# Performance work log

Hardware: AMD Instinct MI355X
Metric: run time of the kernel (lower is better)

## Reference

```python
import jax, jax.numpy as jnp
import numpy as np

B, T, E, H = 4, 2048, 1024, 16
HS = E // H  # 64
EPS = 1e-5


def _layernorm(x, g, b):
    mu = jnp.mean(x, axis=-1, keepdims=True)
    var = jnp.mean(jnp.square(x - mu), axis=-1, keepdims=True)
    return (x - mu) * jax.lax.rsqrt(var + EPS) * g + b


def setup_inputs() -> dict:
    key = jax.random.key(0)
    ks = jax.random.split(key, 12)
    s = 0.02
    return {
        "x": jax.random.normal(ks[0], (B, T, E), dtype=jnp.float32),
        "ln1_g": jnp.ones((E,), jnp.float32),
        "ln1_b": jnp.zeros((E,), jnp.float32),
        "Wq": jax.random.normal(ks[1], (H, E, HS), jnp.float32) * s,
        "Wk": jax.random.normal(ks[2], (H, E, HS), jnp.float32) * s,
        "Wv": jax.random.normal(ks[3], (H, E, HS), jnp.float32) * s,
        "Wo": jax.random.normal(ks[4], (E, E), jnp.float32) * s,
        "bo": jnp.zeros((E,), jnp.float32),
        "ln2_g": jnp.ones((E,), jnp.float32),
        "ln2_b": jnp.zeros((E,), jnp.float32),
        "W1": jax.random.normal(ks[5], (E, 4 * E), jnp.float32) * s,
        "b1": jnp.zeros((4 * E,), jnp.float32),
        "W2": jax.random.normal(ks[6], (4 * E, E), jnp.float32) * s,
        "b2": jnp.zeros((E,), jnp.float32),
    }


def reference(x, ln1_g, ln1_b, Wq, Wk, Wv, Wo, bo, ln2_g, ln2_b, W1, b1, W2, b2):
    # --- self-attention (pre-LN) ---
    h = _layernorm(x, ln1_g, ln1_b)                      # [B,T,E]
    q = jnp.einsum('bte,hed->bhtd', h, Wq)               # [B,H,T,HS]
    k = jnp.einsum('bte,hed->bhtd', h, Wk)
    v = jnp.einsum('bte,hed->bhtd', h, Wv)
    scores = jnp.einsum('bhtd,bhsd->bhts', q, k) * (HS ** -0.5)  # [B,H,T,T]
    att = jax.nn.softmax(scores, axis=-1)
    o = jnp.einsum('bhts,bhsd->bhtd', att, v)            # [B,H,T,HS]
    o = jnp.transpose(o, (0, 2, 1, 3)).reshape(B, T, E)  # concat heads
    x = x + o @ Wo + bo                                  # residual
    # --- feed-forward (pre-LN) ---
    h2 = _layernorm(x, ln2_g, ln2_b)
    x = x + jax.nn.relu(h2 @ W1 + b1) @ W2 + b2
    return x
```

## Files before the change

### kernel.cpp

```cpp
#include <hip/hip_runtime.h>
#include <stdint.h>


typedef __attribute__((ext_vector_type(8))) short s16x8;
typedef __attribute__((ext_vector_type(4))) float f32x4;
typedef unsigned short u16;
typedef __attribute__((ext_vector_type(4))) unsigned short u16x4;

__device__ __forceinline__ u16 f2bf(float f) {
    uint32_t u = __float_as_uint(f);
    u += 0x7fffu + ((u >> 16) & 1u);
    return (u16)(u >> 16);
}

__global__ __launch_bounds__(256)
void ln_bf16(const float* __restrict__ x, const float* __restrict__ g,
             const float* __restrict__ bta, u16* __restrict__ y) {
    __shared__ float red[8];
    const int row = blockIdx.x;
    const int t = threadIdx.x;
    const float4 xv = ((const float4*)(x + (size_t)row * 1024))[t];
    float s = xv.x + xv.y + xv.z + xv.w;
    float q = xv.x*xv.x + xv.y*xv.y + xv.z*xv.z + xv.w*xv.w;
#pragma unroll
    for (int off = 32; off; off >>= 1) {
        s += __shfl_down(s, off, 64);
        q += __shfl_down(q, off, 64);
    }
    if ((t & 63) == 0) { red[(t>>6)*2] = s; red[(t>>6)*2+1] = q; }
    __syncthreads();
    const float st = red[0]+red[2]+red[4]+red[6];
    const float qt = red[1]+red[3]+red[5]+red[7];
    const float mu = st * (1.f/1024.f);
    const float rs = rsqrtf(qt*(1.f/1024.f) - mu*mu + 1e-5f);
    const float4 gv = ((const float4*)g)[t];
    const float4 bv = ((const float4*)bta)[t];
    u16x4 o;
    o.x = f2bf((xv.x-mu)*rs*gv.x + bv.x);
    o.y = f2bf((xv.y-mu)*rs*gv.y + bv.y);
    o.z = f2bf((xv.z-mu)*rs*gv.z + bv.z);
    o.w = f2bf((xv.w-mu)*rs*gv.w + bv.w);
    ((u16x4*)(y + (size_t)row*1024))[t] = o;
}

__global__ __launch_bounds__(256)
void transpose_f32_bf16(const float* __restrict__ in, u16* __restrict__ out,
                        int K, int N) {
    __shared__ float tile[64][65];
    const int k0 = blockIdx.x * 64;
    const int n0 = blockIdx.y * 64;
    const int t = threadIdx.x;
    const int r = t >> 2;
    const int c = (t & 3) * 16;
    const float* ip = in + (size_t)(k0 + r) * N + n0 + c;
#pragma unroll
    for (int i = 0; i < 4; ++i) {
        const float4 v = *(const float4*)(ip + i*4);
        tile[r][c+i*4+0]=v.x; tile[r][c+i*4+1]=v.y;
        tile[r][c+i*4+2]=v.z; tile[r][c+i*4+3]=v.w;
    }
    __syncthreads();
    u16 tmp[16] __attribute__((aligned(16)));
#pragma unroll
    for (int i = 0; i < 16; ++i) tmp[i] = f2bf(tile[c+i][r]);
    u16* op = out + (size_t)(n0 + r) * K + k0 + c;
    *(s16x8*)op       = *(const s16x8*)&tmp[0];
    *(s16x8*)(op + 8) = *(const s16x8*)&tmp[8];
}

__global__ __launch_bounds__(256)
void pack_wcat(const float* __restrict__ Wq, const float* __restrict__ Wk,
               const float* __restrict__ Wv, u16* __restrict__ out) {
    __shared__ float tile[64][65];
    const int ph = blockIdx.y;
    const int p = ph >> 4, h = ph & 15;
    const float* W = (p == 0) ? Wq : (p == 1 ? Wk : Wv);
    const float* in = W + (size_t)h * 64 * 1024;
    const int k0 = blockIdx.x * 64;
    const int t = threadIdx.x;
    const int r = t >> 2;
    const int c = (t & 3) * 16;
    const float* ip = in + (size_t)(k0 + r) * 64 + c;
#pragma unroll
    for (int i = 0; i < 4; ++i) {
        const float4 v = *(const float4*)(ip + i*4);
        tile[r][c+i*4+0]=v.x; tile[r][c+i*4+1]=v.y;
        tile[r][c+i*4+2]=v.z; tile[r][c+i*4+3]=v.w;
    }
    __syncthreads();
    u16 tmp[16] __attribute__((aligned(16)));
#pragma unroll
    for (int i = 0; i < 16; ++i) tmp[i] = f2bf(tile[c+i][r]);
    u16* op = out + (size_t)(p*1024 + h*64 + r) * 1024 + k0 + c;
    *(s16x8*)op       = *(const s16x8*)&tmp[0];
    *(s16x8*)(op + 8) = *(const s16x8*)&tmp[8];
}

template<bool RELU, bool HAS_BIAS, bool HAS_RES, bool OUT_BF16>
__global__ __launch_bounds__(256, 2)
void bgemm(const u16* __restrict__ A, int lda,
           const u16* __restrict__ Bt, int ldb,
           void* __restrict__ Cv, int ldc,
           const float* __restrict__ bias,
           const float* __restrict__ Res, int ldres, int K)
{
    __shared__ u16 Als[128*64];
    __shared__ u16 Bls[128*64];
    const int tid = threadIdx.x;
    const int wid = tid >> 6, lane = tid & 63;
    const int bm = blockIdx.y * 128, bn = blockIdx.x * 128;
    const int wr = (wid >> 1) * 64, wc = (wid & 1) * 64;
    const int srow = tid >> 3;
    const int sce  = (tid & 7) * 8;
    const int fr = lane & 15, fq = lane >> 4;

    const f32x4 zero = {0.f, 0.f, 0.f, 0.f};
    f32x4 acc[4][4];
#pragma unroll
    for (int m = 0; m < 4; ++m)
#pragma unroll
        for (int n = 0; n < 4; ++n) acc[m][n] = zero;

    const u16* Ap = A  + (size_t)(bm + srow) * lda + sce;
    const u16* Bp = Bt + (size_t)(bn + srow) * ldb + sce;
    const size_t a32 = (size_t)32 * lda, b32 = (size_t)32 * ldb;

    int wb[4];
#pragma unroll
    for (int c2 = 0; c2 < 4; ++c2) {
        const int row = c2*32 + srow;
        wb[c2] = row*128 + (((tid & 7) * 16) ^ ((row & 7) << 4));
    }

    s16x8 ar[4], br[4];
#pragma unroll
    for (int c2 = 0; c2 < 4; ++c2) {
        ar[c2] = *(const s16x8*)(Ap + c2*a32);
        br[c2] = *(const s16x8*)(Bp + c2*b32);
    }

    for (int k0 = 0; k0 < K; k0 += 64) {
        __syncthreads();
#pragma unroll
        for (int c2 = 0; c2 < 4; ++c2) {
            *(s16x8*)((char*)Als + wb[c2]) = ar[c2];
            *(s16x8*)((char*)Bls + wb[c2]) = br[c2];
        }
        __syncthreads();
        if (k0 + 64 < K) {
#pragma unroll
            for (int c2 = 0; c2 < 4; ++c2) {
                ar[c2] = *(const s16x8*)(Ap + (k0 + 64) + c2*a32);
                br[c2] = *(const s16x8*)(Bp + (k0 + 64) + c2*b32);
            }
        }
#pragma unroll
        for (int kk = 0; kk < 2; ++kk) {
            s16x8 af[4], bf[4];
#pragma unroll
            for (int m = 0; m < 4; ++m) {
                const int r = wr + m*16 + fr;
                const int cb = (kk*64 + fq*16) ^ ((r & 7) << 4);
                af[m] = *(const s16x8*)((const char*)Als + r*128 + cb);
            }
#pragma unroll
            for (int n = 0; n < 4; ++n) {
                const int r = wc + n*16 + fr;
                const int cb = (kk*64 + fq*16) ^ ((r & 7) << 4);
                bf[n] = *(const s16x8*)((const char*)Bls + r*128 + cb);
            }
#pragma unroll
            for (int m = 0; m < 4; ++m)
#pragma unroll
                for (int n = 0; n < 4; ++n)
                    acc[m][n] = __builtin_amdgcn_mfma_f32_16x16x32_bf16(
                        af[m], bf[n], acc[m][n], 0, 0, 0);
        }
    }

    float* Cf = (float*)Cv;
    u16*  Cb = (u16*)Cv;
#pragma unroll
    for (int n = 0; n < 4; ++n) {
        const int col = bn + wc + n*16 + fr;
        const float bval = HAS_BIAS ? bias[col] : 0.f;
#pragma unroll
        for (int m = 0; m < 4; ++m) {
#pragma unroll
            for (int j = 0; j < 4; ++j) {
                const int row = bm + wr + m*16 + fq*4 + j;
                float v = acc[m][n][j] + bval;
                if (HAS_RES) v += Res[(size_t)row * ldres + col];
                if (RELU)    v = fmaxf(v, 0.f);
                if (OUT_BF16) Cb[(size_t)row * ldc + col] = f2bf(v);
                else          Cf[(size_t)row * ldc + col] = v;
            }
        }
    }
}

__global__ __launch_bounds__(256)
void attn_bf16(const u16* __restrict__ qkv, u16* __restrict__ out) {
    __shared__ u16 Qs[64*72];
    __shared__ u16 Ks[64*72];
    __shared__ u16 Vt[64*72];
    __shared__ u16 Ps[64*72];
    const int b = blockIdx.y >> 4, h = blockIdx.y & 15;
    const int q0 = blockIdx.x << 6;
    const int tid = threadIdx.x;
    const int wid = tid >> 6, lane = tid & 63;
    const int fr = lane & 15, fq = lane >> 4;
    const int srow = tid >> 2;
    const int sce  = (tid & 3) * 16;
    const size_t tokbase = (size_t)b * 2048;

    {
        const u16* qp = qkv + (tokbase + q0 + srow) * 3072 + h*64 + sce;
        *(s16x8*)&Qs[srow*72 + sce]     = *(const s16x8*)qp;
        *(s16x8*)&Qs[srow*72 + sce + 8] = *(const s16x8*)(qp + 8);
    }
    const s16x8 qf0 = *(const s16x8*)&Qs[(wid*16 + fr)*72 + fq*8];
    const s16x8 qf1 = *(const s16x8*)&Qs[(wid*16 + fr)*72 + 32 + fq*8];

    float m_run[4] = {-3e38f, -3e38f, -3e38f, -3e38f};
    float l_run[4] = {0.f, 0.f, 0.f, 0.f};
    const f32x4 zero = {0.f, 0.f, 0.f, 0.f};
    f32x4 oacc[4];
#pragma unroll
    for (int nd = 0; nd < 4; ++nd) oacc[nd] = zero;

    for (int kt = 0; kt < 2048; kt += 64) {
        const u16* kp = qkv + (tokbase + kt + srow)*3072 + 1024 + h*64 + sce;
        const s16x8 kv0 = *(const s16x8*)kp;
        const s16x8 kv1 = *(const s16x8*)(kp + 8);
        const s16x8 vv0 = *(const s16x8*)(kp + 1024);
        const s16x8 vv1 = *(const s16x8*)(kp + 1032);
        __syncthreads();
        *(s16x8*)&Ks[srow*72 + sce]     = kv0;
        *(s16x8*)&Ks[srow*72 + sce + 8] = kv1;
#pragma unroll
        for (int i = 0; i < 8; ++i) {
            Vt[(sce + i)*72 + srow]     = (u16)vv0[i];
            Vt[(sce + i + 8)*72 + srow] = (u16)vv1[i];
        }
        __syncthreads();

        f32x4 sv[4];
#pragma unroll
        for (int n = 0; n < 4; ++n) sv[n] = zero;
#pragma unroll
        for (int n = 0; n < 4; ++n) {
            const s16x8 kf0 = *(const s16x8*)&Ks[(n*16 + fr)*72 + fq*8];
            const s16x8 kf1 = *(const s16x8*)&Ks[(n*16 + fr)*72 + 32 + fq*8];
            sv[n] = __builtin_amdgcn_mfma_f32_16x16x32_bf16(qf0, kf0, sv[n], 0,0,0);
            sv[n] = __builtin_amdgcn_mfma_f32_16x16x32_bf16(qf1, kf1, sv[n], 0,0,0);
        }

#pragma unroll
        for (int j = 0; j < 4; ++j) {
            const float s0 = sv[0][j]*0.125f, s1 = sv[1][j]*0.125f;
            const float s2 = sv[2][j]*0.125f, s3 = sv[3][j]*0.125f;
            float mx = fmaxf(fmaxf(s0, s1), fmaxf(s2, s3));
#pragma unroll
            for (int off = 1; off < 16; off <<= 1)
                mx = fmaxf(mx, __shfl_xor(mx, off, 64));
            const float mn = fmaxf(m_run[j], mx);
            const float al = __expf(m_run[j] - mn);
            m_run[j] = mn;
            const float p0 = __expf(s0 - mn), p1 = __expf(s1 - mn);
            const float p2 = __expf(s2 - mn), p3 = __expf(s3 - mn);
            float rs = p0 + p1 + p2 + p3;
#pragma unroll
            for (int off = 1; off < 16; off <<= 1)
                rs += __shfl_xor(rs, off, 64);
            l_run[j] = l_run[j]*al + rs;
#pragma unroll
            for (int nd = 0; nd < 4; ++nd) oacc[nd][j] *= al;
            const int prow = (wid*16 + fq*4 + j)*72;
            Ps[prow + fr]      = f2bf(p0);
            Ps[prow + 16 + fr] = f2bf(p1);
            Ps[prow + 32 + fr] = f2bf(p2);
            Ps[prow + 48 + fr] = f2bf(p3);
        }

        const s16x8 pf0 = *(const s16x8*)&Ps[(wid*16 + fr)*72 + fq*8];
        const s16x8 pf1 = *(const s16x8*)&Ps[(wid*16 + fr)*72 + 32 + fq*8];
#pragma unroll
        for (int nd = 0; nd < 4; ++nd) {
            const s16x8 vf0 = *(const s16x8*)&Vt[(nd*16 + fr)*72 + fq*8];
            const s16x8 vf1 = *(const s16x8*)&Vt[(nd*16 + fr)*72 + 32 + fq*8];
            oacc[nd] = __builtin_amdgcn_mfma_f32_16x16x32_bf16(pf0, vf0, oacc[nd], 0,0,0);
            oacc[nd] = __builtin_amdgcn_mfma_f32_16x16x32_bf16(pf1, vf1, oacc[nd], 0,0,0);
        }
    }

#pragma unroll
    for (int j = 0; j < 4; ++j) {
        const float inv = 1.0f / l_run[j];
        const size_t row = tokbase + q0 + wid*16 + fq*4 + j;
#pragma unroll
        for (int nd = 0; nd < 4; ++nd)
            out[row*1024 + h*64 + nd*16 + fr] = f2bf(oacc[nd][j] * inv);
    }
}

extern "C" void kernel_launch(void* const* d_in, const int* in_sizes, int n_in,
                              void* d_out, int out_size, void* d_ws, size_t ws_size,
                              hipStream_t stream) {
    (void)in_sizes; (void)n_in; (void)out_size; (void)ws_size;
    const float* x     = (const float*)d_in[0];
    const float* ln1_g = (const float*)d_in[1];
    const float* ln1_b = (const float*)d_in[2];
    const float* Wq    = (const float*)d_in[3];
    const float* Wk    = (const float*)d_in[4];
    const float* Wv    = (const float*)d_in[5];
    const float* Wo    = (const float*)d_in[6];
    const float* bo    = (const float*)d_in[7];
    const float* ln2_g = (const float*)d_in[8];
    const float* ln2_b = (const float*)d_in[9];
    const float* W1    = (const float*)d_in[10];
    const float* b1    = (const float*)d_in[11];
    const float* W2    = (const float*)d_in[12];
    const float* b2    = (const float*)d_in[13];
    float* out = (float*)d_out;

    char* w = (char*)d_ws;
    u16* WcatT = (u16*)w;  w += (size_t)3072*1024*2;
    u16* WoT   = (u16*)w;  w += (size_t)1024*1024*2;
    u16* W1T   = (u16*)w;  w += (size_t)4096*1024*2;
    u16* W2T   = (u16*)w;  w += (size_t)1024*4096*2;
    u16* hb    = (u16*)w;  w += (size_t)8192*1024*2;
    u16* qkvb  = (u16*)w;  w += (size_t)8192*3072*2;
    u16* attno = (u16*)w;  w += (size_t)8192*1024*2;
    u16* a1    = (u16*)w;  w += (size_t)8192*4096*2;

    pack_wcat<<<dim3(16, 48), 256, 0, stream>>>(Wq, Wk, Wv, WcatT);
    transpose_f32_bf16<<<dim3(16, 16), 256, 0, stream>>>(Wo, WoT, 1024, 1024);
    transpose_f32_bf16<<<dim3(16, 64), 256, 0, stream>>>(W1, W1T, 1024, 4096);
    transpose_f32_bf16<<<dim3(64, 16), 256, 0, stream>>>(W2, W2T, 4096, 1024);

    ln_bf16<<<dim3(8192), 256, 0, stream>>>(x, ln1_g, ln1_b, hb);
    bgemm<false,false,false,true><<<dim3(24, 64), 256, 0, stream>>>(
        hb, 1024, WcatT, 1024, qkvb, 3072, nullptr, nullptr, 0, 1024);
    attn_bf16<<<dim3(32, 64), 256, 0, stream>>>(qkvb, attno);
    bgemm<false,true,true,false><<<dim3(8, 64), 256, 0, stream>>>(
        attno, 1024, WoT, 1024, out, 1024, bo, x, 1024, 1024);
    ln_bf16<<<dim3(8192), 256, 0, stream>>>(out, ln2_g, ln2_b, hb);
    bgemm<true,true,false,true><<<dim3(32, 64), 256, 0, stream>>>(
        hb, 1024, W1T, 1024, a1, 4096, b1, nullptr, 0, 1024);
    bgemm<false,true,true,false><<<dim3(8, 64), 256, 0, stream>>>(
        a1, 4096, W2T, 4096, out, 1024, b2, out, 1024, 4096);
}
```

Baseline: 718.0 us.

## Use direct global-to-LDS loads in GEMM and restructure attention with transposed scores

The GEMM now loads A/B tiles straight into LDS with global_load_lds, dropping the register staging, the XOR swizzle and the register prefetch, and relaxes launch bounds. Attention moves to 128-key tiles with swizzled LDS layouts and computes S^T (K times Q), so each lane owns a single query row. This removes most of the cross-lane shuffles in the softmax, and the 1/8 scale is folded into Q once. The aim is less LDS bank conflict and reduction overhead in attention and less staging cost in the GEMM, but the GEMM loses its load/compute overlap and may now see unswizzled LDS read conflicts.

New measurement: 634.6 us. 1.13x faster.

```diff
diff --git a/kernel.cpp b/kernel.cpp
--- a/kernel.cpp
+++ b/kernel.cpp
@@ -7,10 +7,24 @@
 typedef unsigned short u16;
 typedef __attribute__((ext_vector_type(4))) unsigned short u16x4;
 
+#define XSW(r) ((((r) & 7) ^ (((r) >> 3) & 7)) << 4)
+
 __device__ __forceinline__ u16 f2bf(float f) {
     uint32_t u = __float_as_uint(f);
     u += 0x7fffu + ((u >> 16) & 1u);
     return (u16)(u >> 16);
+}
+__device__ __forceinline__ float bf2f(u16 u) {
+    return __uint_as_float(((uint32_t)u) << 16);
+}
+__device__ __forceinline__ uint32_t pk2(float a, float b) {
+    return (uint32_t)f2bf(a) | ((uint32_t)f2bf(b) << 16);
+}
+
+__device__ __forceinline__ void gld16(const void* g, void* l) {
+    __builtin_amdgcn_global_load_lds(
+        (const __attribute__((address_space(1))) unsigned int*)g,
+        (__attribute__((address_space(3))) unsigned int*)l, 16, 0, 0);
 }
 
 __global__ __launch_bounds__(256)
@@ -97,12 +111,12 @@
 }
 
 template<bool RELU, bool HAS_BIAS, bool HAS_RES, bool OUT_BF16>
-__global__ __launch_bounds__(256, 2)
+__global__ __launch_bounds__(256)
 void bgemm(const u16* __restrict__ A, int lda,
            const u16* __restrict__ Bt, int ldb,
-           void* __restrict__ Cv, int ldc,
+           void* Cv, int ldc,
            const float* __restrict__ bias,
-           const float* __restrict__ Res, int ldres, int K)
+           const float* Res, int ldres, int K)
 {
     __shared__ u16 Als[128*64];
     __shared__ u16 Bls[128*64];
@@ -110,9 +124,8 @@
     const int wid = tid >> 6, lane = tid & 63;
     const int bm = blockIdx.y * 128, bn = blockIdx.x * 128;
     const int wr = (wid >> 1) * 64, wc = (wid & 1) * 64;
-    const int srow = tid >> 3;
-    const int sce  = (tid & 7) * 8;
     const int fr = lane & 15, fq = lane >> 4;
+    const int sr8 = lane >> 3, sc8 = (lane & 7) * 8;
 
     const f32x4 zero = {0.f, 0.f, 0.f, 0.f};
     f32x4 acc[4][4];
@@ -121,54 +134,27 @@
 #pragma unroll
         for (int n = 0; n < 4; ++n) acc[m][n] = zero;
 
-    const u16* Ap = A  + (size_t)(bm + srow) * lda + sce;
-    const u16* Bp = Bt + (size_t)(bn + srow) * ldb + sce;
-    const size_t a32 = (size_t)32 * lda, b32 = (size_t)32 * ldb;
-
-    int wb[4];
-#pragma unroll
-    for (int c2 = 0; c2 < 4; ++c2) {
-        const int row = c2*32 + srow;
-        wb[c2] = row*128 + (((tid & 7) * 16) ^ ((row & 7) << 4));
-    }
-
-    s16x8 ar[4], br[4];
-#pragma unroll
-    for (int c2 = 0; c2 < 4; ++c2) {
-        ar[c2] = *(const s16x8*)(Ap + c2*a32);
-        br[c2] = *(const s16x8*)(Bp + c2*b32);
-    }
+    const u16* Ap = A  + (size_t)(bm + wid*32 + sr8) * lda + sc8;
+    const u16* Bp = Bt + (size_t)(bn + wid*32 + sr8) * ldb + sc8;
+    u16* Alp = Als + wid*2048 + lane*8;
+    u16* Blp = Bls + wid*2048 + lane*8;
 
     for (int k0 = 0; k0 < K; k0 += 64) {
+#pragma unroll
+        for (int c = 0; c < 4; ++c) {
+            gld16(Ap + (size_t)(c*8)*lda + k0, Alp + c*512);
+            gld16(Bp + (size_t)(c*8)*ldb + k0, Blp + c*512);
+        }
         __syncthreads();
-#pragma unroll
-        for (int c2 = 0; c2 < 4; ++c2) {
-            *(s16x8*)((char*)Als + wb[c2]) = ar[c2];
-            *(s16x8*)((char*)Bls + wb[c2]) = br[c2];
-        }
-        __syncthreads();
-        if (k0 + 64 < K) {
-#pragma unroll
-            for (int c2 = 0; c2 < 4; ++c2) {
-                ar[c2] = *(const s16x8*)(Ap + (k0 + 64) + c2*a32);
-                br[c2] = *(const s16x8*)(Bp + (k0 + 64) + c2*b32);
-            }
-        }
 #pragma unroll
         for (int kk = 0; kk < 2; ++kk) {
             s16x8 af[4], bf[4];
 #pragma unroll
-            for (int m = 0; m < 4; ++m) {
-                const int r = wr + m*16 + fr;
-                const int cb = (kk*64 + fq*16) ^ ((r & 7) << 4);
-                af[m] = *(const s16x8*)((const char*)Als + r*128 + cb);
-            }
-#pragma unroll
-            for (int n = 0; n < 4; ++n) {
-                const int r = wc + n*16 + fr;
-                const int cb = (kk*64 + fq*16) ^ ((r & 7) << 4);
-                bf[n] = *(const s16x8*)((const char*)Bls + r*128 + cb);
-            }
+            for (int m = 0; m < 4; ++m)
+                af[m] = *(const s16x8*)((const char*)Als + (wr+m*16+fr)*128 + kk*64 + fq*16);
+#pragma unroll
+            for (int n = 0; n < 4; ++n)
+                bf[n] = *(const s16x8*)((const char*)Bls + (wc+n*16+fr)*128 + kk*64 + fq*16);
 #pragma unroll
             for (int m = 0; m < 4; ++m)
 #pragma unroll
@@ -176,6 +162,7 @@
                     acc[m][n] = __builtin_amdgcn_mfma_f32_16x16x32_bf16(
                         af[m], bf[n], acc[m][n], 0, 0, 0);
         }
+        __syncthreads();
     }
 
     float* Cf = (float*)Cv;
@@ -201,10 +188,9 @@
 
 __global__ __launch_bounds__(256)
 void attn_bf16(const u16* __restrict__ qkv, u16* __restrict__ out) {
-    __shared__ u16 Qs[64*72];
-    __shared__ u16 Ks[64*72];
-    __shared__ u16 Vt[64*72];
-    __shared__ u16 Ps[64*72];
+    __shared__ u16 Ks[128*64];
+    __shared__ u16 Vt[64*128];
+    __shared__ u16 Ps[4][16*128];
     const int b = blockIdx.y >> 4, h = blockIdx.y & 15;
     const int q0 = blockIdx.x << 6;
     const int tid = threadIdx.x;
@@ -213,94 +199,138 @@
     const int srow = tid >> 2;
     const int sce  = (tid & 3) * 16;
     const size_t tokbase = (size_t)b * 2048;
-
+    const f32x4 zero = {0.f, 0.f, 0.f, 0.f};
+
+    u16* Qst = (u16*)Ps;
     {
-        const u16* qp = qkv + (tokbase + q0 + srow) * 3072 + h*64 + sce;
-        *(s16x8*)&Qs[srow*72 + sce]     = *(const s16x8*)qp;
-        *(s16x8*)&Qs[srow*72 + sce + 8] = *(const s16x8*)(qp + 8);
-    }
-    const s16x8 qf0 = *(const s16x8*)&Qs[(wid*16 + fr)*72 + fq*8];
-    const s16x8 qf1 = *(const s16x8*)&Qs[(wid*16 + fr)*72 + 32 + fq*8];
-
-    float m_run[4] = {-3e38f, -3e38f, -3e38f, -3e38f};
-    float l_run[4] = {0.f, 0.f, 0.f, 0.f};
-    const f32x4 zero = {0.f, 0.f, 0.f, 0.f};
+        const u16* qp = qkv + (tokbase + q0 + srow)*3072 + h*64 + sce;
+        const s16x8 v0 = *(const s16x8*)qp;
+        const s16x8 v1 = *(const s16x8*)(qp + 8);
+        *(s16x8*)((char*)Qst + srow*128 + ((sce*2)      ^ XSW(srow))) = v0;
+        *(s16x8*)((char*)Qst + srow*128 + ((sce*2 + 16) ^ XSW(srow))) = v1;
+    }
+    __syncthreads();
+    s16x8 qf[2];
+    {
+        const int qrow = wid*16 + fr;
+#pragma unroll
+        for (int kk = 0; kk < 2; ++kk) {
+            const s16x8 raw = *(const s16x8*)((const char*)Qst + qrow*128
+                                 + ((kk*64 + fq*16) ^ XSW(qrow)));
+#pragma unroll
+            for (int i = 0; i < 8; ++i)
+                qf[kk][i] = (short)f2bf(bf2f((u16)raw[i]) * 0.125f);
+        }
+    }
+
+    float m_run = -1e30f, l_run = 0.f;
     f32x4 oacc[4];
 #pragma unroll
     for (int nd = 0; nd < 4; ++nd) oacc[nd] = zero;
 
-    for (int kt = 0; kt < 2048; kt += 64) {
-        const u16* kp = qkv + (tokbase + kt + srow)*3072 + 1024 + h*64 + sce;
-        const s16x8 kv0 = *(const s16x8*)kp;
-        const s16x8 kv1 = *(const s16x8*)(kp + 8);
-        const s16x8 vv0 = *(const s16x8*)(kp + 1024);
-        const s16x8 vv1 = *(const s16x8*)(kp + 1032);
+    for (int kt = 0; kt < 2048; kt += 128) {
+        const u16* kp0 = qkv + (tokbase + kt + srow)*3072 + 1024 + h*64 + sce;
+        const u16* kp1 = kp0 + (size_t)64*3072;
+        const s16x8 ka0 = *(const s16x8*)kp0;
+        const s16x8 ka1 = *(const s16x8*)(kp0 + 8);
+        const s16x8 kb0 = *(const s16x8*)kp1;
+        const s16x8 kb1 = *(const s16x8*)(kp1 + 8);
+        const s16x8 va0 = *(const s16x8*)(kp0 + 1024);
+        const s16x8 va1 = *(const s16x8*)(kp0 + 1032);
+        const s16x8 vb0 = *(const s16x8*)(kp1 + 1024);
+        const s16x8 vb1 = *(const s16x8*)(kp1 + 1032);
         __syncthreads();
-        *(s16x8*)&Ks[srow*72 + sce]     = kv0;
-        *(s16x8*)&Ks[srow*72 + sce + 8] = kv1;
+        {
+            const int r0 = srow, r1 = srow + 64;
+            *(s16x8*)((char*)Ks + r0*128 + ((sce*2)      ^ XSW(r0))) = ka0;
+            *(s16x8*)((char*)Ks + r0*128 + ((sce*2 + 16) ^ XSW(r0))) = ka1;
+            *(s16x8*)((char*)Ks + r1*128 + ((sce*2)      ^ XSW(r1))) = kb0;
+            *(s16x8*)((char*)Ks + r1*128 + ((sce*2 + 16) ^ XSW(r1))) = kb1;
+        }
 #pragma unroll
         for (int i = 0; i < 8; ++i) {
-            Vt[(sce + i)*72 + srow]     = (u16)vv0[i];
-            Vt[(sce + i + 8)*72 + srow] = (u16)vv1[i];
+            const int d0 = sce + i, d1 = sce + 8 + i;
+            *(u16*)((char*)Vt + d0*256 + ((srow*2)        ^ XSW(d0))) = (u16)va0[i];
+            *(u16*)((char*)Vt + d1*256 + ((srow*2)        ^ XSW(d1))) = (u16)va1[i];
+            *(u16*)((char*)Vt + d0*256 + (((srow+64)*2)   ^ XSW(d0))) = (u16)vb0[i];
+            *(u16*)((char*)Vt + d1*256 + (((srow+64)*2)   ^ XSW(d1))) = (u16)vb1[i];
         }
         __syncthreads();
 
-        f32x4 sv[4];
-#pragma unroll
-        for (int n = 0; n < 4; ++n) sv[n] = zero;
-#pragma unroll
-        for (int n = 0; n < 4; ++n) {
-            const s16x8 kf0 = *(const s16x8*)&Ks[(n*16 + fr)*72 + fq*8];
-            const s16x8 kf1 = *(const s16x8*)&Ks[(n*16 + fr)*72 + 32 + fq*8];
-            sv[n] = __builtin_amdgcn_mfma_f32_16x16x32_bf16(qf0, kf0, sv[n], 0,0,0);
-            sv[n] = __builtin_amdgcn_mfma_f32_16x16x32_bf16(qf1, kf1, sv[n], 0,0,0);
-        }
-
-#pragma unroll
-        for (int j = 0; j < 4; ++j) {
-            const float s0 = sv[0][j]*0.125f, s1 = sv[1][j]*0.125f;
-            const float s2 = sv[2][j]*0.125f, s3 = sv[3][j]*0.125f;
-            float mx = fmaxf(fmaxf(s0, s1), fmaxf(s2, s3));
-#pragma unroll
-            for (int off = 1; off < 16; off <<= 1)
-                mx = fmaxf(mx, __shfl_xor(mx, off, 64));
-            const float mn = fmaxf(m_run[j], mx);
-            const float al = __expf(m_run[j] - mn);
-            m_run[j] = mn;
-            const float p0 = __expf(s0 - mn), p1 = __expf(s1 - mn);
-            const float p2 = __expf(s2 - mn), p3 = __expf(s3 - mn);
-            float rs = p0 + p1 + p2 + p3;
-#pragma unroll
-            for (int off = 1; off < 16; off <<= 1)
-                rs += __shfl_xor(rs, off, 64);
-            l_run[j] = l_run[j]*al + rs;
-#pragma unroll
-            for (int nd = 0; nd < 4; ++nd) oacc[nd][j] *= al;
-            const int prow = (wid*16 + fq*4 + j)*72;
-            Ps[prow + fr]      = f2bf(p0);
-            Ps[prow + 16 + fr] = f2bf(p1);
-            Ps[prow + 32 + fr] = f2bf(p2);
-            Ps[prow + 48 + fr] = f2bf(p3);
-        }
-
-        const s16x8 pf0 = *(const s16x8*)&Ps[(wid*16 + fr)*72 + fq*8];
-        const s16x8 pf1 = *(const s16x8*)&Ps[(wid*16 + fr)*72 + 32 + fq*8];
+        f32x4 sv[8];
+#pragma unroll
+        for (int n = 0; n < 8; ++n) {
+            sv[n] = zero;
+            const int r = n*16 + fr;
+#pragma unroll
+            for (int kk = 0; kk < 2; ++kk) {
+                const s16x8 kf = *(const s16x8*)((const char*)Ks + r*128
+                                     + ((kk*64 + fq*16) ^ XSW(r)));
+                sv[n] = __builtin_amdgcn_mfma_f32_16x16x32_bf16(kf, qf[kk], sv[n], 0,0,0);
+            }
+        }
+
+        float pv[32];
+        float mx = -1e30f;
+#pragma unroll
+        for (int n = 0; n < 8; ++n)
+#pragma unroll
+            for (int j = 0; j < 4; ++j) {
+                const float s = sv[n][j];
+                pv[n*4 + j] = s;
+                mx = fmaxf(mx, s);
+            }
+        mx = fmaxf(mx, __shfl_xor(mx, 16, 64));
+        mx = fmaxf(mx, __shfl_xor(mx, 32, 64));
+        const float mn = fmaxf(m_run, mx);
+        const float al = __expf(m_run - mn);
+        m_run = mn;
+        float rs = 0.f;
+#pragma unroll
+        for (int t = 0; t < 32; ++t) { pv[t] = __expf(pv[t] - mn); rs += pv[t]; }
+        rs += __shfl_xor(rs, 16, 64);
+        rs += __shfl_xor(rs, 32, 64);
+        l_run = l_run * al + rs;
+#pragma unroll
+        for (int nd = 0; nd < 4; ++nd)
+#pragma unroll
+            for (int j = 0; j < 4; ++j) oacc[nd][j] *= al;
+
+        u16* Pw = (u16*)Ps + wid*2048;
+#pragma unroll
+        for (int n = 0; n < 8; ++n) {
+            const uint64_t w = (uint64_t)pk2(pv[n*4+0], pv[n*4+1])
+                             | ((uint64_t)pk2(pv[n*4+2], pv[n*4+3]) << 32);
+            *(uint64_t*)((char*)Pw + fr*256 + ((n*32 + fq*8) ^ XSW(fr))) = w;
+        }
+        asm volatile("s_waitcnt lgkmcnt(0)" ::: "memory");
+        __builtin_amdgcn_sched_barrier(0);
+
+        s16x8 pf[4];
+#pragma unroll
+        for (int k2 = 0; k2 < 4; ++k2)
+            pf[k2] = *(const s16x8*)((const char*)Pw + fr*256
+                         + ((k2*64 + fq*16) ^ XSW(fr)));
 #pragma unroll
         for (int nd = 0; nd < 4; ++nd) {
-            const s16x8 vf0 = *(const s16x8*)&Vt[(nd*16 + fr)*72 + fq*8];
-            const s16x8 vf1 = *(const s16x8*)&Vt[(nd*16 + fr)*72 + 32 + fq*8];
-            oacc[nd] = __builtin_amdgcn_mfma_f32_16x16x32_bf16(pf0, vf0, oacc[nd], 0,0,0);
-            oacc[nd] = __builtin_amdgcn_mfma_f32_16x16x32_bf16(pf1, vf1, oacc[nd], 0,0,0);
-        }
-    }
-
-#pragma unroll
-    for (int j = 0; j < 4; ++j) {
-        const float inv = 1.0f / l_run[j];
-        const size_t row = tokbase + q0 + wid*16 + fq*4 + j;
-#pragma unroll
-        for (int nd = 0; nd < 4; ++nd)
-            out[row*1024 + h*64 + nd*16 + fr] = f2bf(oacc[nd][j] * inv);
+            const int d = nd*16 + fr;
+#pragma unroll
+            for (int k2 = 0; k2 < 4; ++k2) {
+                const s16x8 vf = *(const s16x8*)((const char*)Vt + d*256
+                                     + ((k2*64 + fq*16) ^ XSW(d)));
+                oacc[nd] = __builtin_amdgcn_mfma_f32_16x16x32_bf16(vf, pf[k2], oacc[nd], 0,0,0);
+            }
+        }
+    }
+
+    const float inv = 1.0f / l_run;
+    const size_t row = tokbase + q0 + wid*16 + fr;
+#pragma unroll
+    for (int nd = 0; nd < 4; ++nd) {
+        u16x4 o;
+#pragma unroll
+        for (int j = 0; j < 4; ++j) o[j] = f2bf(oacc[nd][j] * inv);
+        *(u16x4*)(out + row*1024 + h*64 + nd*16 + fq*4) = o;
     }
 }
 
```
